# Kernel tuning notes

Measured on AMD Instinct MI355X. Metric: run time of the kernel, lower is better.

The kernel has to match this reference:

```python
import jax, jax.numpy as jnp
import numpy as np

N, E = 50000, 800000
IN_F, HID, OUT_F, K = 128, 128, 64, 3
LAMBDA_MAX = 2.0  # standard upper bound for normalized-Laplacian eigenvalues (dgl.laplacian_lambda_max)
BN_EPS = 1e-5


def setup_inputs() -> dict:
    key = jax.random.key(0)
    ks = jax.random.split(key, 8)
    s = 0.05
    features = jax.random.normal(ks[0], (N, IN_F), jnp.float32)
    src = jax.random.randint(ks[1], (E,), 0, N)
    dst = jax.random.randint(ks[2], (E,), 0, N)
    W1 = jax.random.normal(ks[3], (HID, K * IN_F), jnp.float32) * s
    b1 = jnp.zeros((HID,), jnp.float32)
    W3 = jax.random.normal(ks[4], (HID, K * HID), jnp.float32) * s
    b3 = jnp.zeros((HID,), jnp.float32)
    gamma = jnp.ones((HID,), jnp.float32)
    beta = jnp.zeros((HID,), jnp.float32)
    Wm1 = jax.random.normal(ks[5], (HID, HID), jnp.float32) * s
    bm1 = jnp.zeros((HID,), jnp.float32)
    Wm2 = jax.random.normal(ks[6], (OUT_F, HID), jnp.float32) * s
    bm2 = jnp.zeros((OUT_F,), jnp.float32)
    return dict(features=features, src=src, dst=dst, W1=W1, b1=b1, W3=W3, b3=b3,
                gamma=gamma, beta=beta, Wm1=Wm1, bm1=bm1, Wm2=Wm2, bm2=bm2)


def chebconv(feat, src, dst, d_invsqrt, W, b, k):
    """DGL ChebConv: T_0 = X, T_1 = Lhat X, T_i = 2 Lhat T_{i-1} - T_{i-2};
    Lhat = (2/lam) (I - Ahat) - I, Ahat = D^{-1/2} A D^{-1/2}; linear over concat of orders."""
    re_norm = 2.0 / LAMBDA_MAX
    n = feat.shape[0]

    def spmv(x):  # Ahat @ x via edge gather (src) + segment-sum scatter (dst)
        return jax.ops.segment_sum((x * d_invsqrt)[src], dst, num_segments=n) * d_invsqrt

    Xs = [feat]
    if k > 1:
        h = spmv(feat)
        Xs.append(-re_norm * h + feat * (re_norm - 1.0))
    for _ in range(2, k):
        h = spmv(Xs[-1])
        Xs.append(-2.0 * re_norm * h + Xs[-1] * (2.0 * (re_norm - 1.0)) - Xs[-2])
    return jnp.concatenate(Xs, axis=1) @ W.T + b  # [N, k*d] @ [d_out, k*d]^T


def reference(features, src, dst, W1, b1, W3, b3, gamma, beta, Wm1, bm1, Wm2, bm2):
    n = features.shape[0]
    in_deg = jax.ops.segment_sum(jnp.ones((src.shape[0],), jnp.float32), dst, num_segments=n)
    d_invsqrt = (jnp.clip(in_deg, 1.0, None) ** -0.5)[:, None]

    x = jax.nn.relu(chebconv(features, src, dst, d_invsqrt, W1, b1, K))
    # BatchNorm1d (training-mode batch stats, biased variance)
    mu = x.mean(axis=0)
    var = x.var(axis=0)
    x = (x - mu) * jax.lax.rsqrt(var + BN_EPS) * gamma + beta
    # NOTE: the source's Chebyshev early-stopping loop computes cheb2(x) repeatedly but
    # never reassigns `x`, so it is output-inert and omitted (same math).
    x_res = x
    x = jax.nn.relu(chebconv(x, src, dst, d_invsqrt, W3, b3, K))
    x = x + x_res  # dropout in eval mode == identity
    h = jax.nn.relu(x @ Wm1.T + bm1)
    return h @ Wm2.T + bm2
```

## Files before the change

### kernel.cpp

```cpp
#include <hip/hip_runtime.h>
#include <hip/hip_bf16.h>
#include <math.h>

#define NF 128

typedef unsigned short ushort8 __attribute__((ext_vector_type(8)));
typedef float f32x4 __attribute__((ext_vector_type(4)));
typedef _Float16 half8 __attribute__((ext_vector_type(8)));

static inline int ceil_div(int a, int b) { return (a + b - 1) / b; }

__global__ __launch_bounds__(256) void bucket_hist_kernel(const int* __restrict__ dst,
                                                          int* __restrict__ counts,
                                                          int e, int nblk, int nbuck) {
  __shared__ int h[256];
  int t = threadIdx.x, blk = blockIdx.x;
  h[t] = 0;
  __syncthreads();
  int base = blk * 4096;
#pragma unroll
  for (int k = 0; k < 16; ++k) {
    int i = base + k * 256 + t;
    if (i < e) atomicAdd(&h[dst[i] >> 8], 1);
  }
  __syncthreads();
  for (int b = t; b < nbuck; b += 256) counts[b * nblk + blk] = h[b];
}

__global__ __launch_bounds__(256) void bucket_scan_rows_kernel(int* __restrict__ counts,
                                                               int* __restrict__ btot,
                                                               int nblk) {
  __shared__ int sh[256];
  int b = blockIdx.x, t = threadIdx.x;
  int* row = counts + (size_t)b * nblk;
  int carry = 0;
  for (int base = 0; base < nblk; base += 256) {
    int v = (base + t < nblk) ? row[base + t] : 0;
    sh[t] = v;
    __syncthreads();
    for (int off = 1; off < 256; off <<= 1) {
      int add = (t >= off) ? sh[t - off] : 0;
      __syncthreads();
      sh[t] += add;
      __syncthreads();
    }
    if (base + t < nblk) row[base + t] = carry + sh[t] - v;
    carry += sh[255];
    __syncthreads();
  }
  if (t == 0) btot[b] = carry;
}

__global__ __launch_bounds__(256) void bucket_bin_kernel(const int* __restrict__ src,
                                                         const int* __restrict__ dst,
                                                         const int* __restrict__ counts,
                                                         const int* __restrict__ btot,
                                                         unsigned int* __restrict__ binned,
                                                         int e, int nblk, int nbuck) {
  __shared__ int sh[256];
  __shared__ int cur[256];
  int t = threadIdx.x, blk = blockIdx.x;
  int v = (t < nbuck) ? btot[t] : 0;
  sh[t] = v;
  __syncthreads();
  for (int off = 1; off < 256; off <<= 1) {
    int add = (t >= off) ? sh[t - off] : 0;
    __syncthreads();
    sh[t] += add;
    __syncthreads();
  }
  if (t < nbuck) cur[t] = counts[(size_t)t * nblk + blk] + (sh[t] - v);
  __syncthreads();
  int base = blk * 4096;
#pragma unroll
  for (int k = 0; k < 16; ++k) {
    int i = base + k * 256 + t;
    if (i < e) {
      int d = dst[i];
      int pos = atomicAdd(&cur[d >> 8], 1);
      binned[pos] = ((unsigned)(d & 255) << 16) | (unsigned)src[i];
    }
  }
}

__global__ __launch_bounds__(256) void bucket_finalize_kernel(const unsigned int* __restrict__ binned,
                                                              const int* __restrict__ btot,
                                                              int* __restrict__ offsets,
                                                              int* __restrict__ csr,
                                                              float* __restrict__ dinv,
                                                              int n, int e, int nbuck) {
  __shared__ int sh[256];
  __shared__ int deg[256];
  __shared__ int offs[256];
  __shared__ int cur[256];
  __shared__ int sbeg, send;
  int b = blockIdx.x, t = threadIdx.x;
  int v0 = (t < nbuck) ? btot[t] : 0;
  sh[t] = v0;
  __syncthreads();
  for (int off = 1; off < 256; off <<= 1) {
    int add = (t >= off) ? sh[t - off] : 0;
    __syncthreads();
    sh[t] += add;
    __syncthreads();
  }
  if (t == 0) { sbeg = (b > 0) ? sh[b - 1] : 0; send = sh[b]; }
  deg[t] = 0;
  __syncthreads();
  int ebeg = sbeg, eend = send;
  for (int j = ebeg + t; j < eend; j += 256) atomicAdd(&deg[binned[j] >> 16], 1);
  __syncthreads();
  int v = deg[t];
  offs[t] = v;
  __syncthreads();
  for (int off = 1; off < 256; off <<= 1) {
    int add = (t >= off) ? offs[t - off] : 0;
    __syncthreads();
    offs[t] += add;
    __syncthreads();
  }
  int excl = offs[t] - v;
  cur[t] = excl;
  int node = b * 256 + t;
  if (node < n) {
    offsets[node] = ebeg + excl;
    float d = (float)(v > 1 ? v : 1);
    dinv[node] = rsqrtf(d);
  }
  if (b == nbuck - 1 && t == 0) offsets[n] = e;
  __syncthreads();
  for (int j = ebeg + t; j < eend; j += 256) {
    unsigned int pr = binned[j];
    int pos = atomicAdd(&cur[pr >> 16], 1);
    csr[ebeg + pos] = (int)(pr & 0xFFFFu);
  }
}


__device__ __forceinline__ void pack_one(const float* __restrict__ W, ushort8* __restrict__ Wp,
                                         int f, int NT, int K, int rot) {
  int lane = f & 63;
  int hl = (f >> 6) & 1;
  int rest = f >> 7;
  int nt = rest % NT;
  int kunit = rest / NT;
  int nK = K >> 5;
  int srcKunit = (kunit + rot) % nK;
  int nrow = nt * 16 + (lane & 15);
  int k0 = srcKunit * 32 + (lane >> 4) * 8;
  const float* srcp = W + (size_t)nrow * K + k0;
  ushort8 v;
#pragma unroll
  for (int j = 0; j < 8; ++j) {
    float x = srcp[j];
    _Float16 h = (_Float16)x;
    if (hl) h = (_Float16)(x - (float)h);
    v[j] = __builtin_bit_cast(unsigned short, h);
  }
  Wp[f] = v;
}

__global__ void prep_pack_kernel(const float* __restrict__ feat, _Float16* __restrict__ Fsp,
                                 int n, int fb,
                                 const float* __restrict__ W1, ushort8* __restrict__ P1,
                                 const float* __restrict__ W3, ushort8* __restrict__ P3,
                                 const float* __restrict__ Wm1, ushort8* __restrict__ PM1,
                                 const float* __restrict__ Wm2, ushort8* __restrict__ PM2) {
  int blk = blockIdx.x;
  if (blk < fb) {
    int i = blk * 256 + threadIdx.x;
    if (i >= n * 16) return;
    int row = i >> 4, fc = i & 15;
    const float4* s = (const float4*)(feat + (size_t)row * NF + fc * 8);
    float4 a = s[0], b = s[1];
    float xv[8] = {a.x, a.y, a.z, a.w, b.x, b.y, b.z, b.w};
    half8 f;
#pragma unroll
    for (int j = 0; j < 8; ++j) f[j] = (_Float16)xv[j];
    int swz = (fc ^ (row & 15)) * 8;
    *(half8*)(Fsp + (size_t)row * 128 + swz) = f;
  } else {
    int f = (blk - fb) * 256 + threadIdx.x;
    if (f < 12288) pack_one(W1, P1, f, 8, 384, 0);
    else if (f < 24576) pack_one(W3, P3, f - 12288, 8, 384, 4);
    else if (f < 28672) pack_one(Wm1, PM1, f - 24576, 8, 128, 0);
    else if (f < 30720) pack_one(Wm2, PM2, f - 28672, 4, 128, 0);
  }
}

__global__ __launch_bounds__(256) void spmv_kernel(
    const _Float16* __restrict__ xsp, const float* __restrict__ dinv,
    const int* __restrict__ offsets, const int* __restrict__ csr,
    const _Float16* __restrict__ zsp, float a, float bz,
    _Float16* __restrict__ outsp, int n) {
  int w = threadIdx.x >> 6, lane = threadIdx.x & 63;
  int node = blockIdx.x * 4 + w;
  if (node >= n) return;
  int beg = __builtin_amdgcn_readfirstlane(offsets[node]);
  int end = __builtin_amdgcn_readfirstlane(offsets[node + 1]);
  int eh = lane >> 4;
  int cq = lane & 15;

  float acc[8];
#pragma unroll
  for (int j = 0; j < 8; ++j) acc[j] = 0.f;

  int e2 = beg;
  for (; e2 + 8 <= end; e2 += 8) {
    int s0 = csr[e2 + eh];
    int s1 = csr[e2 + 4 + eh];
    float w0 = dinv[s0], w1 = dinv[s1];
    half8 g0 = *(const half8*)(xsp + (size_t)s0 * 128 + ((cq ^ (s0 & 15)) << 3));
    half8 g1 = *(const half8*)(xsp + (size_t)s1 * 128 + ((cq ^ (s1 & 15)) << 3));
#pragma unroll
    for (int j = 0; j < 8; ++j) acc[j] += w0 * (float)g0[j];
#pragma unroll
    for (int j = 0; j < 8; ++j) acc[j] += w1 * (float)g1[j];
  }
  for (; e2 + 4 <= end; e2 += 4) {
    int s0 = csr[e2 + eh];
    float w0 = dinv[s0];
    half8 g0 = *(const half8*)(xsp + (size_t)s0 * 128 + ((cq ^ (s0 & 15)) << 3));
#pragma unroll
    for (int j = 0; j < 8; ++j) acc[j] += w0 * (float)g0[j];
  }
  int rem = end - e2;
  if (eh < rem) {
    int s0 = csr[e2 + eh];
    float w0 = dinv[s0];
    half8 g0 = *(const half8*)(xsp + (size_t)s0 * 128 + ((cq ^ (s0 & 15)) << 3));
#pragma unroll
    for (int j = 0; j < 8; ++j) acc[j] += w0 * (float)g0[j];
  }
#pragma unroll
  for (int j = 0; j < 8; ++j) {
    acc[j] += __shfl_xor(acc[j], 16);
    acc[j] += __shfl_xor(acc[j], 32);
  }
  if (eh == 0) {
    float dv = a * dinv[node];
    float v[8];
#pragma unroll
    for (int j = 0; j < 8; ++j) v[j] = dv * acc[j];
    int swz = (cq ^ (node & 15)) << 3;
    if (zsp) {
      half8 zz = *(const half8*)(zsp + (size_t)node * 128 + swz);
#pragma unroll
      for (int j = 0; j < 8; ++j) v[j] += bz * (float)zz[j];
    }
    half8 ho;
#pragma unroll
    for (int j = 0; j < 8; ++j) ho[j] = (_Float16)v[j];
    *(half8*)(outsp + (size_t)node * 128 + swz) = ho;
  }
}


__device__ __forceinline__ void stage_sp(const _Float16* gsrc, float4* lbuf, int tid) {
  const char* g = (const char*)gsrc;
  char* l = (char*)lbuf;
#pragma unroll
  for (int k = 0; k < 2; ++k) {
    int off = k * 8192 + tid * 16;
    __builtin_amdgcn_global_load_lds(
        (const __attribute__((address_space(1))) void*)(g + off),
        (__attribute__((address_space(3))) void*)(l + off), 16, 0, 0);
  }
}

__device__ __forceinline__ int lds_off16(int row, int col) {
  return row * 128 + (((col >> 3) ^ (row & 15)) << 3) + (col & 7);
}

struct Bchunk {
  ushort8 h[2][2];
  ushort8 l[2][2];
};

__device__ __forceinline__ void loadB(const ushort8* __restrict__ Wp, int kunit0,
                                      int lane, int wn, Bchunk& c) {
#pragma unroll
  for (int k2 = 0; k2 < 2; ++k2) {
#pragma unroll
    for (int j = 0; j < 2; ++j) {
      const ushort8* bp = Wp + (size_t)((kunit0 + k2) * 8 + wn * 2 + j) * 128 + lane;
      c.h[k2][j] = bp[0];
      c.l[k2][j] = bp[64];
    }
  }
}

__device__ __forceinline__ void mfma_chunk(const float4* A4, const Bchunk& c, int kbase,
                                           int lane, int wm, f32x4 (*acc)[2]) {
#pragma unroll
  for (int k2 = 0; k2 < 2; ++k2) {
    int kunit = kbase + k2;
    half8 a[2];
#pragma unroll
    for (int mt = 0; mt < 2; ++mt) {
      int arow = wm * 32 + mt * 16 + (lane & 15);
      int fc = (kunit & 3) * 4 + (lane >> 4);
      a[mt] = __builtin_bit_cast(half8, A4[arow * 16 + (fc ^ (arow & 15))]);
    }
#pragma unroll
    for (int j = 0; j < 2; ++j) {
      half8 bh = __builtin_bit_cast(half8, c.h[k2][j]);
      half8 bl = __builtin_bit_cast(half8, c.l[k2][j]);
#pragma unroll
      for (int mt = 0; mt < 2; ++mt) {
        acc[mt][j] = __builtin_amdgcn_mfma_f32_16x16x32_f16(a[mt], bh, acc[mt][j], 0, 0, 0);
        acc[mt][j] = __builtin_amdgcn_mfma_f32_16x16x32_f16(a[mt], bl, acc[mt][j], 0, 0, 0);
      }
    }
  }
}

template<int NT, int NT2>
__device__ __forceinline__ void gemm_step16(const float4* A4, const ushort8* __restrict__ Wp,
                                            int kunit, int lane, int wm, int wn,
                                            f32x4 (*acc)[NT2]) {
  half8 a[2];
#pragma unroll
  for (int mt = 0; mt < 2; ++mt) {
    int arow = wm * 32 + mt * 16 + (lane & 15);
    int fc = (kunit & 3) * 4 + (lane >> 4);
    a[mt] = __builtin_bit_cast(half8, A4[arow * 16 + (fc ^ (arow & 15))]);
  }
#pragma unroll
  for (int j = 0; j < NT2; ++j) {
    int nt = wn * NT2 + j;
    const ushort8* bp = Wp + (size_t)(kunit * NT + nt) * 2 * 64 + lane;
    half8 bh = __builtin_bit_cast(half8, bp[0]);
    half8 bl = __builtin_bit_cast(half8, bp[64]);
#pragma unroll
    for (int mt = 0; mt < 2; ++mt) {
      acc[mt][j] = __builtin_amdgcn_mfma_f32_16x16x32_f16(a[mt], bh, acc[mt][j], 0, 0, 0);
      acc[mt][j] = __builtin_amdgcn_mfma_f32_16x16x32_f16(a[mt], bl, acc[mt][j], 0, 0, 0);
    }
  }
}

__device__ __forceinline__ void gemm3_single(const _Float16* A0, const _Float16* A1,
                                             const _Float16* A2, const ushort8* Wp,
                                             float4* lds, size_t r0,
                                             int tid, int lane, int wm, int wn,
                                             f32x4 (*acc)[2]) {
  stage_sp(A0 + r0 * 128, lds, tid);
  stage_sp(A1 + r0 * 128, lds + 1024, tid);
  stage_sp(A2 + r0 * 128, lds + 2048, tid);
  Bchunk bc0, bc1;
  loadB(Wp, 0, lane, wn, bc0);
  asm volatile("s_waitcnt vmcnt(8)" ::: "memory");
  __builtin_amdgcn_s_barrier();
  __builtin_amdgcn_sched_barrier(0);
  loadB(Wp, 2, lane, wn, bc1);
  mfma_chunk(lds, bc0, 0, lane, wm, acc);
  loadB(Wp, 4, lane, wn, bc0);
  mfma_chunk(lds, bc1, 2, lane, wm, acc);
  loadB(Wp, 6, lane, wn, bc1);
  mfma_chunk(lds + 1024, bc0, 4, lane, wm, acc);
  loadB(Wp, 8, lane, wn, bc0);
  mfma_chunk(lds + 1024, bc1, 6, lane, wm, acc);
  loadB(Wp, 10, lane, wn, bc1);
  mfma_chunk(lds + 2048, bc0, 8, lane, wm, acc);
  mfma_chunk(lds + 2048, bc1, 10, lane, wm, acc);
}

__global__ __launch_bounds__(512, 4) void conv1_gemm_kernel(
    const _Float16* __restrict__ A0, const _Float16* __restrict__ A1,
    const _Float16* __restrict__ A2,
    const ushort8* __restrict__ Wp, const float* __restrict__ bias,
    _Float16* __restrict__ Xsp, float* __restrict__ stats, int n) {
  __shared__ float4 lds[3072];
  __shared__ float sstat[256];

  int tid = threadIdx.x;
  int lane = tid & 63, wid = tid >> 6;
  int wm = wid >> 2, wn = wid & 3;
  size_t r0 = (size_t)blockIdx.x * 64;

  f32x4 acc[2][2];
#pragma unroll
  for (int mt = 0; mt < 2; ++mt)
#pragma unroll
    for (int j = 0; j < 2; ++j) acc[mt][j] = (f32x4)0.f;

  gemm3_single(A0, A1, A2, Wp, lds, r0, tid, lane, wm, wn, acc);

  if (tid < 256) sstat[tid] = 0.f;
  __syncthreads();
#pragma unroll
  for (int mt = 0; mt < 2; ++mt) {
    int rbase = (int)r0 + wm * 32 + mt * 16 + (lane >> 4) * 4;
#pragma unroll
    for (int j = 0; j < 2; ++j) {
      int col = wn * 32 + j * 16 + (lane & 15);
      float b = bias[col];
      float sj = 0.f, qj = 0.f;
#pragma unroll
      for (int i = 0; i < 4; ++i) {
        int row = rbase + i;
        if (row < n) {
          float v = fmaxf(acc[mt][j][i] + b, 0.f);
          Xsp[(size_t)row * 128 + (((col >> 3) ^ (row & 15)) << 3) + (col & 7)] = (_Float16)v;
          sj += v; qj += v * v;
        }
      }
      sj += __shfl_xor(sj, 16); sj += __shfl_xor(sj, 32);
      qj += __shfl_xor(qj, 16); qj += __shfl_xor(qj, 32);
      if ((lane >> 4) == 0) {
        atomicAdd(&sstat[col], sj);
        atomicAdd(&sstat[128 + col], qj);
      }
    }
  }
  __syncthreads();
  if (tid < 256) atomicAdd(&stats[(blockIdx.x & 7) * 256 + tid], sstat[tid]);
}

__global__ __launch_bounds__(512, 4) void fused_tail_kernel(
    const _Float16* __restrict__ T1sp, const _Float16* __restrict__ T2sp,
    const _Float16* __restrict__ Xsp,
    const ushort8* __restrict__ Wp3, const float* __restrict__ b3,
    const ushort8* __restrict__ WpM1, const float* __restrict__ bm1,
    const ushort8* __restrict__ WpM2, const float* __restrict__ bm2,
    float* __restrict__ out, int n) {
  __shared__ float4 lds[3072];
  _Float16* L0 = (_Float16*)lds;
  _Float16* LX = (_Float16*)(lds + 2048);

  int tid = threadIdx.x;
  int lane = tid & 63, wid = tid >> 6;
  int wm = wid >> 2, wn = wid & 3;
  size_t r0 = (size_t)blockIdx.x * 64;

  f32x4 acc[2][2];
#pragma unroll
  for (int mt = 0; mt < 2; ++mt)
#pragma unroll
    for (int j = 0; j < 2; ++j) acc[mt][j] = (f32x4)0.f;

  gemm3_single(T1sp, T2sp, Xsp, Wp3, lds, r0, tid, lane, wm, wn, acc);
  __syncthreads();

#pragma unroll
  for (int mt = 0; mt < 2; ++mt) {
    int rb = wm * 32 + mt * 16 + (lane >> 4) * 4;
#pragma unroll
    for (int j = 0; j < 2; ++j) {
      int col = wn * 32 + j * 16 + (lane & 15);
      float b = b3[col];
#pragma unroll
      for (int i = 0; i < 4; ++i) {
        int lrow = rb + i;
        int off = lds_off16(lrow, col);
        float xres = (float)LX[off];
        float v = fmaxf(acc[mt][j][i] + b, 0.f) + xres;
        L0[off] = (_Float16)v;
      }
    }
  }
  __syncthreads();
  f32x4 acc2[2][2];
#pragma unroll
  for (int mt = 0; mt < 2; ++mt)
#pragma unroll
    for (int j = 0; j < 2; ++j) acc2[mt][j] = (f32x4)0.f;
#pragma unroll
  for (int ks = 0; ks < 4; ++ks)
    gemm_step16<8, 2>(lds, WpM1, ks, lane, wm, wn, acc2);
  __syncthreads();
#pragma unroll
  for (int mt = 0; mt < 2; ++mt) {
    int rb = wm * 32 + mt * 16 + (lane >> 4) * 4;
#pragma unroll
    for (int j = 0; j < 2; ++j) {
      int col = wn * 32 + j * 16 + (lane & 15);
      float b = bm1[col];
#pragma unroll
      for (int i = 0; i < 4; ++i) {
        float v = fmaxf(acc2[mt][j][i] + b, 0.f);
        L0[lds_off16(rb + i, col)] = (_Float16)v;
      }
    }
  }
  __syncthreads();
  f32x4 acc3[2][1];
#pragma unroll
  for (int mt = 0; mt < 2; ++mt) acc3[mt][0] = (f32x4)0.f;
#pragma unroll
  for (int ks = 0; ks < 4; ++ks)
    gemm_step16<4, 1>(lds, WpM2, ks, lane, wm, wn, acc3);
#pragma unroll
  for (int mt = 0; mt < 2; ++mt) {
    int rb = wm * 32 + mt * 16 + (lane >> 4) * 4;
    int col = wn * 16 + (lane & 15);
    float b = bm2[col];
#pragma unroll
    for (int i = 0; i < 4; ++i) {
      int row = (int)r0 + rb + i;
      if (row < n) out[(size_t)row * 64 + col] = acc3[mt][0][i] + b;
    }
  }
}

__global__ void bn_apply_kernel(_Float16* __restrict__ Xsp, const float* __restrict__ stats,
                                const float* __restrict__ gamma, const float* __restrict__ beta,
                                float fn, int n) {
  int i = blockIdx.x * 256 + threadIdx.x;
  if (i >= n * 16) return;
  int row = i >> 4, fc = i & 15;
  int swz = (fc ^ (row & 15)) * 8;
  half8* xp = (half8*)(Xsp + (size_t)row * 128 + swz);
  half8 xh = *xp;
  half8 hu;
  int c0 = fc * 8;
#pragma unroll
  for (int j = 0; j < 8; ++j) {
    int c = c0 + j;
    float s1 = 0.f, s2 = 0.f;
#pragma unroll
    for (int r = 0; r < 8; ++r) {
      s1 += stats[r * 256 + c];
      s2 += stats[r * 256 + NF + c];
    }
    float mu = s1 / fn;
    float var = s2 / fn - mu * mu;
    float s = gamma[c] * rsqrtf(var + 1e-5f);
    hu[j] = (_Float16)(((float)xh[j] - mu) * s + beta[c]);
  }
  *xp = hu;
}

extern "C" void kernel_launch(void* const* d_in, const int* in_sizes, int n_in,
                              void* d_out, int out_size, void* d_ws, size_t ws_size,
                              hipStream_t stream) {
  const float* feat  = (const float*)d_in[0];
  const int*   src   = (const int*)d_in[1];
  const int*   dst   = (const int*)d_in[2];
  const float* W1    = (const float*)d_in[3];
  const float* b1    = (const float*)d_in[4];
  const float* W3    = (const float*)d_in[5];
  const float* b3    = (const float*)d_in[6];
  const float* gamma = (const float*)d_in[7];
  const float* beta  = (const float*)d_in[8];
  const float* Wm1   = (const float*)d_in[9];
  const float* bm1   = (const float*)d_in[10];
  const float* Wm2   = (const float*)d_in[11];
  const float* bm2   = (const float*)d_in[12];
  int n = in_sizes[0] / NF;
  int e = in_sizes[1];

  char* p = (char*)d_ws;
  auto alloc = [&](size_t bytes) {
    char* r = p;
    p += (bytes + 255) & ~size_t(255);
    return r;
  };
  int nblk  = ceil_div(e, 4096);
  int nbuck = ceil_div(n, 256);

  float* dinv     = (float*)alloc((size_t)n * 4);
  int*   offsets  = (int*)alloc((size_t)(n + 1) * 4);
  int*   counts   = (int*)alloc((size_t)nblk * nbuck * 4);
  int*   btot     = (int*)alloc((size_t)nbuck * 4);
  int*   csr      = (int*)alloc((size_t)e * 4);
  float* stats    = (float*)alloc(8 * 256 * 4);
  ushort8* Wp1  = (ushort8*)alloc(12 * 8 * 2 * 64 * 16);
  ushort8* Wp3  = (ushort8*)alloc(12 * 8 * 2 * 64 * 16);
  ushort8* WpM1 = (ushort8*)alloc(4 * 8 * 2 * 64 * 16);
  ushort8* WpM2 = (ushort8*)alloc(4 * 4 * 2 * 64 * 16);
  size_t spb = (size_t)(n + 64) * 256;
  _Float16* Fsp  = (_Float16*)alloc(spb);
  _Float16* T1sp = (_Float16*)alloc(spb);
  _Float16* T2sp = (_Float16*)alloc(spb);
  _Float16* Xsp  = (_Float16*)alloc(spb);
  unsigned int* binned = (unsigned int*)Fsp;

  hipMemsetAsync(stats, 0, 8 * 256 * 4, stream);

  int fb = ceil_div(n * 16, 256);
  int sb = ceil_div(n, 4);
  int gb = ceil_div(n, 64);

  bucket_hist_kernel<<<nblk, 256, 0, stream>>>(dst, counts, e, nblk, nbuck);
  bucket_scan_rows_kernel<<<nbuck, 256, 0, stream>>>(counts, btot, nblk);
  bucket_bin_kernel<<<nblk, 256, 0, stream>>>(src, dst, counts, btot, binned, e, nblk, nbuck);
  bucket_finalize_kernel<<<nbuck, 256, 0, stream>>>(binned, btot, offsets, csr, dinv, n, e, nbuck);

  prep_pack_kernel<<<fb + 120, 256, 0, stream>>>(feat, Fsp, n, fb,
                                                 W1, Wp1, W3, Wp3, Wm1, WpM1, Wm2, WpM2);

  spmv_kernel<<<sb, 256, 0, stream>>>(Fsp, dinv, offsets, csr, nullptr, -1.f, 0.f, T1sp, n);
  spmv_kernel<<<sb, 256, 0, stream>>>(T1sp, dinv, offsets, csr, Fsp, -2.f, -1.f, T2sp, n);
  conv1_gemm_kernel<<<gb, 512, 0, stream>>>(Fsp, T1sp, T2sp, Wp1, b1, Xsp, stats, n);

  bn_apply_kernel<<<fb, 256, 0, stream>>>(Xsp, stats, gamma, beta, (float)n, n);

  spmv_kernel<<<sb, 256, 0, stream>>>(Xsp, dinv, offsets, csr, nullptr, -1.f, 0.f, T1sp, n);
  spmv_kernel<<<sb, 256, 0, stream>>>(T1sp, dinv, offsets, csr, Xsp, -2.f, -1.f, T2sp, n);

  fused_tail_kernel<<<gb, 512, 0, stream>>>(T1sp, T2sp, Xsp, Wp3, b3, WpM1, bm1,
                                            WpM2, bm2, (float*)d_out, n);
}
```

Measured before the change: 251.7 us.

## Fold Chebyshev recurrence coefficients into packed weights, store raw A-hat powers

With lambda_max=2, T1 = -AX and T2 = 2A(AX) - X, so the SpMV kernels now store plain AX and A(AX). The -1, 2 and -X terms are folded into the packed GEMM weights as W0-W2, -W1 and 2*W2. This removes the second SpMV's read of the z operand and the affine epilogue. The cost is slightly different fp16 rounding of intermediate values, and the result is only correct because re_norm equals 1.

```diff
diff --git a/kernel.cpp b/kernel.cpp
--- a/kernel.cpp
+++ b/kernel.cpp
@@ -138,7 +138,7 @@
 
 
 __device__ __forceinline__ void pack_one(const float* __restrict__ W, ushort8* __restrict__ Wp,
-                                         int f, int NT, int K, int rot) {
+                                         int f, int NT, int K, int rot, bool cheb) {
   int lane = f & 63;
   int hl = (f >> 6) & 1;
   int rest = f >> 7;
@@ -146,6 +146,7 @@
   int kunit = rest / NT;
   int nK = K >> 5;
   int srcKunit = (kunit + rot) % nK;
+  int blkid = srcKunit >> 2;
   int nrow = nt * 16 + (lane & 15);
   int k0 = srcKunit * 32 + (lane >> 4) * 8;
   const float* srcp = W + (size_t)nrow * K + k0;
@@ -153,6 +154,11 @@
 #pragma unroll
   for (int j = 0; j < 8; ++j) {
     float x = srcp[j];
+    if (cheb) {
+      if (blkid == 0)      x = x - srcp[j + 256];
+      else if (blkid == 1) x = -x;
+      else                 x = 2.f * x;
+    }
     _Float16 h = (_Float16)x;
     if (hl) h = (_Float16)(x - (float)h);
     v[j] = __builtin_bit_cast(unsigned short, h);
@@ -181,17 +187,16 @@
     *(half8*)(Fsp + (size_t)row * 128 + swz) = f;
   } else {
     int f = (blk - fb) * 256 + threadIdx.x;
-    if (f < 12288) pack_one(W1, P1, f, 8, 384, 0);
-    else if (f < 24576) pack_one(W3, P3, f - 12288, 8, 384, 4);
-    else if (f < 28672) pack_one(Wm1, PM1, f - 24576, 8, 128, 0);
-    else if (f < 30720) pack_one(Wm2, PM2, f - 28672, 4, 128, 0);
+    if (f < 12288) pack_one(W1, P1, f, 8, 384, 0, true);
+    else if (f < 24576) pack_one(W3, P3, f - 12288, 8, 384, 4, true);
+    else if (f < 28672) pack_one(Wm1, PM1, f - 24576, 8, 128, 0, false);
+    else if (f < 30720) pack_one(Wm2, PM2, f - 28672, 4, 128, 0, false);
   }
 }
 
 __global__ __launch_bounds__(256) void spmv_kernel(
     const _Float16* __restrict__ xsp, const float* __restrict__ dinv,
     const int* __restrict__ offsets, const int* __restrict__ csr,
-    const _Float16* __restrict__ zsp, float a, float bz,
     _Float16* __restrict__ outsp, int n) {
   int w = threadIdx.x >> 6, lane = threadIdx.x & 63;
   int node = blockIdx.x * 4 + w;
@@ -238,19 +243,11 @@
     acc[j] += __shfl_xor(acc[j], 32);
   }
   if (eh == 0) {
-    float dv = a * dinv[node];
-    float v[8];
-#pragma unroll
-    for (int j = 0; j < 8; ++j) v[j] = dv * acc[j];
+    float dv = dinv[node];
+    half8 ho;
+#pragma unroll
+    for (int j = 0; j < 8; ++j) ho[j] = (_Float16)(dv * acc[j]);
     int swz = (cq ^ (node & 15)) << 3;
-    if (zsp) {
-      half8 zz = *(const half8*)(zsp + (size_t)node * 128 + swz);
-#pragma unroll
-      for (int j = 0; j < 8; ++j) v[j] += bz * (float)zz[j];
-    }
-    half8 ho;
-#pragma unroll
-    for (int j = 0; j < 8; ++j) ho[j] = (_Float16)v[j];
     *(half8*)(outsp + (size_t)node * 128 + swz) = ho;
   }
 }
@@ -591,14 +588,14 @@
   prep_pack_kernel<<<fb + 120, 256, 0, stream>>>(feat, Fsp, n, fb,
                                                  W1, Wp1, W3, Wp3, Wm1, WpM1, Wm2, WpM2);
 
-  spmv_kernel<<<sb, 256, 0, stream>>>(Fsp, dinv, offsets, csr, nullptr, -1.f, 0.f, T1sp, n);
-  spmv_kernel<<<sb, 256, 0, stream>>>(T1sp, dinv, offsets, csr, Fsp, -2.f, -1.f, T2sp, n);
+  spmv_kernel<<<sb, 256, 0, stream>>>(Fsp, dinv, offsets, csr, T1sp, n);
+  spmv_kernel<<<sb, 256, 0, stream>>>(T1sp, dinv, offsets, csr, T2sp, n);
   conv1_gemm_kernel<<<gb, 512, 0, stream>>>(Fsp, T1sp, T2sp, Wp1, b1, Xsp, stats, n);
 
   bn_apply_kernel<<<fb, 256, 0, stream>>>(Xsp, stats, gamma, beta, (float)n, n);
 
-  spmv_kernel<<<sb, 256, 0, stream>>>(Xsp, dinv, offsets, csr, nullptr, -1.f, 0.f, T1sp, n);
-  spmv_kernel<<<sb, 256, 0, stream>>>(T1sp, dinv, offsets, csr, Xsp, -2.f, -1.f, T2sp, n);
+  spmv_kernel<<<sb, 256, 0, stream>>>(Xsp, dinv, offsets, csr, T1sp, n);
+  spmv_kernel<<<sb, 256, 0, stream>>>(T1sp, dinv, offsets, csr, T2sp, n);
 
   fused_tail_kernel<<<gb, 512, 0, stream>>>(T1sp, T2sp, Xsp, Wp3, b3, WpM1, bm1,
                                             WpM2, bm2, (float*)d_out, n);
```

Result: no change. 247.2 us (-1.8%).
